# Performance work log

Hardware: AMD Instinct MI355X
Metric: run time of the kernel (lower is better)

## Reference

```python
import jax, jax.numpy as jnp
import numpy as np

N = 50000        # nodes
DEG = 16         # fixed out-degree per row (CSR)
E = N * DEG      # edges
H = 4            # attention heads
D = 32           # head feature dim
NEG_SLOPE = 0.2  # GAT leaky-relu slope (scalar hyperparam from forward args)


def setup_inputs() -> dict:
    key = jax.random.key(0)
    k1, k2, k3, k4 = jax.random.split(key, 4)
    attn_row = jax.random.normal(k1, (N, H), dtype=jnp.float32)   # a_dst . Wh_i per head
    attn_col = jax.random.normal(k2, (N, H), dtype=jnp.float32)   # a_src . Wh_j per head
    in_feat = jax.random.normal(k3, (N, H, D), dtype=jnp.float32)  # transformed node feats
    col_indices = jax.random.randint(k4, (E,), 0, N, dtype=jnp.int32)
    row_indptr = (jnp.arange(N + 1, dtype=jnp.int32) * DEG)        # CSR pointers, fixed degree
    return {
        "attn_row": attn_row,
        "attn_col": attn_col,
        "in_feat": in_feat,
        "row_indptr": row_indptr,
        "col_indices": col_indices,
    }


def reference(attn_row, attn_col, in_feat, row_indptr, col_indices):
    # Fused GAT: per-edge score = leaky_relu(attn_row[i] + attn_col[j]),
    # softmax over each destination row's edges, then weighted sparse aggregation.
    n = attn_row.shape[0]
    e = col_indices.shape[0]
    # row id of each edge from CSR indptr (jit-safe, static edge count)
    row_ids = jnp.searchsorted(row_indptr, jnp.arange(e, dtype=row_indptr.dtype), side="right") - 1
    score = jax.nn.leaky_relu(attn_row[row_ids] + attn_col[col_indices], NEG_SLOPE)  # [E,H]
    # numerically-stable edge softmax per destination row
    m = jax.ops.segment_max(score, row_ids, num_segments=n)        # [N,H]
    ex = jnp.exp(score - m[row_ids])                               # [E,H]
    denom = jax.ops.segment_sum(ex, row_ids, num_segments=n)       # [N,H]
    alpha = ex / denom[row_ids]                                    # [E,H]
    # gather neighbor features, weight, scatter-add to destinations
    msg = alpha[:, :, None] * in_feat[col_indices]                 # [E,H,D]
    out = jax.ops.segment_sum(msg, row_ids, num_segments=n)        # [N,H,D]
    return out
```

## Files before the change

kernel.cpp:

```cpp
#include <hip/hip_runtime.h>
#include <hip/hip_fp16.h>
#include <math.h>


#define GAT_H 4
#define GAT_D 32
#define GAT_DEG 16
#define GAT_NEG_SLOPE 0.2f

struct alignas(8) half4 { __half2 lo, hi; };

__global__ __launch_bounds__(256) void gat_cvt_kernel(
    const float4* __restrict__ in,
    half4*        __restrict__ outp,
    int n)
{
    const int t = blockIdx.x * 256 + threadIdx.x;
    const int h = blockIdx.y;
    if (t < n * 8) {
        const int nn = t >> 3, q = t & 7;
        const float4 v = in[(nn * GAT_H + h) * 8 + q];
        half4 o;
        o.lo = __floats2half2_rn(v.x, v.y);
        o.hi = __floats2half2_rn(v.z, v.w);
        outp[(size_t)h * n * 8 + t] = o;
    }
}

template <bool FP16>
__global__ __launch_bounds__(256, 4) void gat_main_kernel(
    const float*   __restrict__ attn_row,
    const float*   __restrict__ attn_col,
    const float2*  __restrict__ feat32,
    const __half2* __restrict__ feat16,
    const int*     __restrict__ row_indptr,
    const int*     __restrict__ col_indices,
    float2*        __restrict__ out,
    int n, int nb)
{
    const int b   = blockIdx.x;
    const int xcd = b & 7;
    const int h   = xcd >> 1;
    const int j   = (b >> 3) * 2 + (xcd & 1);
    if (j >= nb) return;

    const int lane = threadIdx.x & 63;
    const int wid  = threadIdx.x >> 6;
    const int g    = lane >> 4;
    const int e    = lane & 15;
    const int dst  = j * 16 + wid * 4 + g;
    if (dst >= n) return;

    const int start = row_indptr[dst];
    const int deg   = row_indptr[dst + 1] - start;

    int idx[GAT_DEG];
    {
        const int4* cip = reinterpret_cast<const int4*>(col_indices + start);
        #pragma unroll
        for (int q = 0; q < 4; ++q) {
            const int4 c = cip[q];
            idx[4*q+0] = c.x; idx[4*q+1] = c.y;
            idx[4*q+2] = c.z; idx[4*q+3] = c.w;
        }
    }

    __half2 hv[GAT_DEG];
    float2  fv[GAT_DEG];
    #pragma unroll
    for (int k = 0; k < GAT_DEG; ++k) {
        if (FP16)
            hv[k] = feat16[((size_t)h * n + idx[k]) * 16 + e];
        else
            fv[k] = feat32[((size_t)idx[k] * GAT_H + h) * 16 + e];
    }
    __builtin_amdgcn_sched_barrier(0);

    const float ar = attn_row[dst * GAT_H + h];
    float s = -INFINITY;
    if (e < deg) {
        const float x = ar + attn_col[idx[e] * GAT_H + h];
        s = (x > 0.0f) ? x : GAT_NEG_SLOPE * x;
    }
    float m = s;
    #pragma unroll
    for (int off = 1; off < 16; off <<= 1)
        m = fmaxf(m, __shfl_xor(m, off));

    const float ex = (e < deg) ? __expf(s - m) : 0.0f;

    float den = ex;
    #pragma unroll
    for (int off = 1; off < 16; off <<= 1)
        den += __shfl_xor(den, off);
    const float rden = __builtin_amdgcn_rcpf(den);

    const int base = lane & 48;
    float accx = 0.0f, accy = 0.0f;
    #pragma unroll
    for (int k = 0; k < GAT_DEG; ++k) {
        const float a = __shfl(ex, base + k);
        const float2 f = FP16 ? __half22float2(hv[k]) : fv[k];
        accx = fmaf(a, f.x, accx);
        accy = fmaf(a, f.y, accy);
    }

    out[((size_t)dst * GAT_H + h) * 16 + e] =
        make_float2(accx * rden, accy * rden);
}

extern "C" void kernel_launch(void* const* d_in, const int* in_sizes, int n_in,
                              void* d_out, int out_size, void* d_ws, size_t ws_size,
                              hipStream_t stream) {
    const float* attn_row    = (const float*)d_in[0];
    const float* attn_col    = (const float*)d_in[1];
    const float* in_feat     = (const float*)d_in[2];
    const int*   row_indptr  = (const int*)d_in[3];
    const int*   col_indices = (const int*)d_in[4];
    float2*      out         = (float2*)d_out;

    const int n      = in_sizes[0] / GAT_H;
    const int n_feat = in_sizes[2];

    const int nb     = (n + 15) / 16;
    const int kmax   = (nb + 1) / 2;
    const int blocks = kmax * 8;

    const size_t fp16_bytes = (size_t)n_feat * sizeof(__half);
    if (ws_size >= fp16_bytes) {
        half4* feat_h = (half4*)d_ws;
        dim3 cgrid((n * 8 + 255) / 256, GAT_H);
        gat_cvt_kernel<<<cgrid, 256, 0, stream>>>(
            (const float4*)in_feat, feat_h, n);
        gat_main_kernel<true><<<blocks, 256, 0, stream>>>(
            attn_row, attn_col, (const float2*)in_feat, (const __half2*)feat_h,
            row_indptr, col_indices, out, n, nb);
    } else {
        gat_main_kernel<false><<<blocks, 256, 0, stream>>>(
            attn_row, attn_col, (const float2*)in_feat, (const __half2*)nullptr,
            row_indptr, col_indices, out, n, nb);
    }
}
```

Before: 125.3 us.

## Switch to node-major fp16 features with one wave per node across all heads

The fp16 conversion now keeps the original node-major layout, using a flat vectorized pass with nontemporal loads. The main kernel maps one wave to each destination node, with 16 lanes per head, so each neighbor gather reads one contiguous 256-byte row for all heads. The output store becomes nontemporal. This drops the XCD-aware per-head block mapping, so each XCD's L2 now sees the whole feature table rather than one head's slice, which risks worse cache locality.

```diff
diff --git a/kernel.cpp b/kernel.cpp
--- a/kernel.cpp
+++ b/kernel.cpp
@@ -9,21 +9,18 @@
 #define GAT_NEG_SLOPE 0.2f
 
 struct alignas(8) half4 { __half2 lo, hi; };
+typedef float floatx4 __attribute__((ext_vector_type(4)));
 
 __global__ __launch_bounds__(256) void gat_cvt_kernel(
-    const float4* __restrict__ in,
-    half4*        __restrict__ outp,
-    int n)
+    const floatx4* __restrict__ in, half4* __restrict__ outp, int n4)
 {
     const int t = blockIdx.x * 256 + threadIdx.x;
-    const int h = blockIdx.y;
-    if (t < n * 8) {
-        const int nn = t >> 3, q = t & 7;
-        const float4 v = in[(nn * GAT_H + h) * 8 + q];
+    if (t < n4) {
+        const floatx4 v = __builtin_nontemporal_load(&in[t]);
         half4 o;
         o.lo = __floats2half2_rn(v.x, v.y);
         o.hi = __floats2half2_rn(v.z, v.w);
-        outp[(size_t)h * n * 8 + t] = o;
+        outp[t] = o;
     }
 }
 
@@ -35,51 +32,46 @@
     const __half2* __restrict__ feat16,
     const int*     __restrict__ row_indptr,
     const int*     __restrict__ col_indices,
-    float2*        __restrict__ out,
-    int n, int nb)
+    float*         __restrict__ out,
+    int n)
 {
-    const int b   = blockIdx.x;
-    const int xcd = b & 7;
-    const int h   = xcd >> 1;
-    const int j   = (b >> 3) * 2 + (xcd & 1);
-    if (j >= nb) return;
+    const int wave_id = (int)((blockIdx.x * (unsigned)blockDim.x + threadIdx.x) >> 6);
+    const int lane    = threadIdx.x & 63;
+    if (wave_id >= n) return;
+    const int dst = wave_id;
+    const int h   = lane >> 4;
+    const int q   = lane & 15;
 
-    const int lane = threadIdx.x & 63;
-    const int wid  = threadIdx.x >> 6;
-    const int g    = lane >> 4;
-    const int e    = lane & 15;
-    const int dst  = j * 16 + wid * 4 + g;
-    if (dst >= n) return;
-
-    const int start = row_indptr[dst];
-    const int deg   = row_indptr[dst + 1] - start;
+    int start = row_indptr[dst];
+    const int deg = row_indptr[dst + 1] - start;
+    start = __builtin_amdgcn_readfirstlane(start);
 
     int idx[GAT_DEG];
     {
         const int4* cip = reinterpret_cast<const int4*>(col_indices + start);
         #pragma unroll
-        for (int q = 0; q < 4; ++q) {
-            const int4 c = cip[q];
-            idx[4*q+0] = c.x; idx[4*q+1] = c.y;
-            idx[4*q+2] = c.z; idx[4*q+3] = c.w;
+        for (int p = 0; p < 4; ++p) {
+            const int4 c = cip[p];
+            idx[4*p+0] = c.x; idx[4*p+1] = c.y;
+            idx[4*p+2] = c.z; idx[4*p+3] = c.w;
         }
     }
+
+    const float ac = attn_col[idx[q] * GAT_H + h];
+    const float ar = attn_row[dst * GAT_H + h];
 
     __half2 hv[GAT_DEG];
     float2  fv[GAT_DEG];
     #pragma unroll
     for (int k = 0; k < GAT_DEG; ++k) {
-        if (FP16)
-            hv[k] = feat16[((size_t)h * n + idx[k]) * 16 + e];
-        else
-            fv[k] = feat32[((size_t)idx[k] * GAT_H + h) * 16 + e];
+        const size_t off = (size_t)idx[k] * (GAT_H * GAT_D / 2) + h * 16 + q;
+        if (FP16) hv[k] = feat16[off];
+        else      fv[k] = feat32[off];
     }
-    __builtin_amdgcn_sched_barrier(0);
 
-    const float ar = attn_row[dst * GAT_H + h];
     float s = -INFINITY;
-    if (e < deg) {
-        const float x = ar + attn_col[idx[e] * GAT_H + h];
+    if (q < deg) {
+        const float x = ar + ac;
         s = (x > 0.0f) ? x : GAT_NEG_SLOPE * x;
     }
     float m = s;
@@ -87,7 +79,7 @@
     for (int off = 1; off < 16; off <<= 1)
         m = fmaxf(m, __shfl_xor(m, off));
 
-    const float ex = (e < deg) ? __expf(s - m) : 0.0f;
+    const float ex = (q < deg) ? __expf(s - m) : 0.0f;
 
     float den = ex;
     #pragma unroll
@@ -99,14 +91,17 @@
     float accx = 0.0f, accy = 0.0f;
     #pragma unroll
     for (int k = 0; k < GAT_DEG; ++k) {
-        const float a = __shfl(ex, base + k);
+        const float a  = __shfl(ex, base + k);
         const float2 f = FP16 ? __half22float2(hv[k]) : fv[k];
         accx = fmaf(a, f.x, accx);
         accy = fmaf(a, f.y, accy);
     }
 
-    out[((size_t)dst * GAT_H + h) * 16 + e] =
-        make_float2(accx * rden, accy * rden);
+    union { float2 f2; double d; } r;
+    r.f2 = make_float2(accx * rden, accy * rden);
+    double* optr = reinterpret_cast<double*>(out) +
+                   ((size_t)dst * GAT_H + h) * 16 + q;
+    __builtin_nontemporal_store(r.d, optr);
 }
 
 extern "C" void kernel_launch(void* const* d_in, const int* in_sizes, int n_in,
@@ -117,27 +112,26 @@
     const float* in_feat     = (const float*)d_in[2];
     const int*   row_indptr  = (const int*)d_in[3];
     const int*   col_indices = (const int*)d_in[4];
-    float2*      out         = (float2*)d_out;
+    float*       out         = (float*)d_out;
 
     const int n      = in_sizes[0] / GAT_H;
     const int n_feat = in_sizes[2];
 
-    const int nb     = (n + 15) / 16;
-    const int kmax   = (nb + 1) / 2;
-    const int blocks = kmax * 8;
+    const int threads = 256;
+    const int blocks  = (n + 3) / 4;
 
     const size_t fp16_bytes = (size_t)n_feat * sizeof(__half);
     if (ws_size >= fp16_bytes) {
         half4* feat_h = (half4*)d_ws;
-        dim3 cgrid((n * 8 + 255) / 256, GAT_H);
-        gat_cvt_kernel<<<cgrid, 256, 0, stream>>>(
-            (const float4*)in_feat, feat_h, n);
-        gat_main_kernel<true><<<blocks, 256, 0, stream>>>(
+        const int n4 = n_feat / 4;
+        gat_cvt_kernel<<<(n4 + 255) / 256, 256, 0, stream>>>(
+            (const floatx4*)in_feat, feat_h, n4);
+        gat_main_kernel<true><<<blocks, threads, 0, stream>>>(
             attn_row, attn_col, (const float2*)in_feat, (const __half2*)feat_h,
-            row_indptr, col_indices, out, n, nb);
+            row_indptr, col_indices, out, n);
     } else {
-        gat_main_kernel<false><<<blocks, 256, 0, stream>>>(
+        gat_main_kernel<false><<<blocks, threads, 0, stream>>>(
             attn_row, attn_col, (const float2*)in_feat, (const __half2*)nullptr,
-            row_indptr, col_indices, out, n, nb);
+            row_indptr, col_indices, out, n);
     }
 }
```

Measured after the change: 117.3 us. -6.4%, faster.
